# Kernel tuning notes

Hardware: AMD Instinct MI355X
Metric: run time of the kernel (lower is better)

The kernel has to match this reference:

```python
import jax, jax.numpy as jnp
import numpy as np

T, B = 32, 64
D_IN = 512      # input_size == embedding dim
H = 512         # hidden_size
V = 32000       # n_vocab
F_FEAT = 768    # feature_size
NH = 8          # num_heads
HD = H // NH    # head_dim


def setup_inputs() -> dict:
    key = jax.random.key(0)
    ks = jax.random.split(key, 16)
    s = 0.02
    inp = {
        'y': jax.random.randint(ks[0], (T, B), 0, V),
        'ctx': jax.random.normal(ks[1], (1, B, F_FEAT), jnp.float32),
        'emb_W': jax.random.normal(ks[2], (V, D_IN), jnp.float32) * s,
        # GRUCell dec0: gates ordered (r, z, n) as in torch
        'W_ih': jax.random.normal(ks[3], (3 * H, D_IN), jnp.float32) * s,
        'b_ih': jnp.zeros((3 * H,), jnp.float32),
        'W_hh': jax.random.normal(ks[4], (3 * H, H), jnp.float32) * s,
        'b_hh': jnp.zeros((3 * H,), jnp.float32),
        # FF att: feature_size -> hidden, tanh
        'W_att': jax.random.normal(ks[5], (H, F_FEAT), jnp.float32) * s,
        'b_att': jnp.zeros((H,), jnp.float32),
        # MultiHeadSelfAttention projections (hidden -> hidden)
        'Wq': jax.random.normal(ks[6], (H, H), jnp.float32) * s,
        'bq': jnp.zeros((H,), jnp.float32),
        'Wk': jax.random.normal(ks[7], (H, H), jnp.float32) * s,
        'bk': jnp.zeros((H,), jnp.float32),
        'Wv': jax.random.normal(ks[8], (H, H), jnp.float32) * s,
        'bv': jnp.zeros((H,), jnp.float32),
        'Wfc': jax.random.normal(ks[9], (H, H), jnp.float32) * s,
        'bfc': jnp.zeros((H,), jnp.float32),
        # FF hid2out: hidden -> input, tanh, bias_zero
        'W_h2o': jax.random.normal(ks[10], (D_IN, H), jnp.float32) * s,
        'b_h2o': jnp.zeros((D_IN,), jnp.float32),
        # FF out2prob: input -> vocab, linear
        'W_out': jax.random.normal(ks[11], (V, D_IN), jnp.float32) * s,
        'b_out': jnp.zeros((V,), jnp.float32),
    }
    return inp


def reference(y, ctx, emb_W, W_ih, b_ih, W_hh, b_hh, W_att, b_att,
              Wq, bq, Wk, bk, Wv, bv, Wfc, bfc, W_h2o, b_h2o, W_out, b_out):
    y_emb = emb_W[y]                                   # [T, B, D_IN]
    # ct is constant across decode steps: tanh FF over pooled image feature
    ct = jnp.tanh(ctx[0] @ W_att.T + b_att)            # [B, H]
    h0 = jnp.zeros((y.shape[1], H), y_emb.dtype)       # dec_init 'zero'

    def step(h, y_t):
        # torch GRUCell (gate order r, z, n)
        gi = y_t @ W_ih.T + b_ih                       # [B, 3H]
        gh = h @ W_hh.T + b_hh                         # [B, 3H]
        gi_r, gi_z, gi_n = jnp.split(gi, 3, axis=-1)
        gh_r, gh_z, gh_n = jnp.split(gh, 3, axis=-1)
        r = jax.nn.sigmoid(gi_r + gh_r)
        z = jax.nn.sigmoid(gi_z + gh_z)
        n = jnp.tanh(gi_n + r * gh_n)
        h1 = (1.0 - z) * n + z * h                     # [B, H]

        x = h1 * ct                                    # [B, H]
        # MultiHeadSelfAttention on a single vector, heads act as sequence
        q = (x @ Wq.T + bq).reshape(-1, NH, HD)        # [B, NH, HD]
        k = (x @ Wk.T + bk).reshape(-1, NH, HD)
        v = (x @ Wv.T + bv).reshape(-1, NH, HD)
        scores = jnp.einsum('bhd,bgd->bhg', q, k) / HD  # note: /head_dim (not sqrt)
        attw = jax.nn.softmax(scores, axis=-1)
        att_out = jnp.einsum('bhg,bgd->bhd', attw, v).reshape(-1, H)
        h2 = att_out @ Wfc.T + bfc                     # [B, H] (fc_out, vocab_size==H)

        logit = jnp.tanh(h2 @ W_h2o.T + b_h2o)         # [B, D_IN]
        prob = jax.nn.softmax(logit @ W_out.T + b_out, axis=-1)  # [B, V]
        return h1, prob                                # f_next returns h1 as next state

    _, probs = jax.lax.scan(step, h0, y_emb)           # [T, B, V]
    return probs
```

## Files before the change

kernel.cpp:

```cpp
#include <hip/hip_runtime.h>
#include <hip/hip_bf16.h>
#include <math.h>

typedef __bf16 bf16_t;
typedef __bf16 bf16x8 __attribute__((ext_vector_type(8)));
typedef __bf16 bf16x4 __attribute__((ext_vector_type(4)));
typedef float  f32x4  __attribute__((ext_vector_type(4)));

#define T_STEPS 32
#define BATCH   64
#define DIN     512
#define HID     512
#define VOCAB   32000
#define FFEAT   768
#define ROWS    2048
#define G3      1536
#define NBLK_A  32

#define EPI_F32  0
#define EPI_BF16 1
#define EPI_TANH 2
#define EPI_SUM  3
#define EPI_PROB 4

#define GLOAD16(gp, lp) __builtin_amdgcn_global_load_lds( \
    (const __attribute__((address_space(1))) void*)(gp),  \
    (__attribute__((address_space(3))) void*)(lp), 16, 0, 0)

template<int EPI>
__global__ __launch_bounds__(256) void gemm_lds(
    const bf16_t* __restrict__ A, const bf16_t* __restrict__ B,
    const float* __restrict__ bias, void* __restrict__ out,
    float* __restrict__ partial, const float* __restrict__ rowsum,
    int M, int N, int K, int NB)
{
  __shared__ bf16_t As[3][128 * 32];
  __shared__ bf16_t Bs[3][128 * 32];
  __shared__ float psum[128][2];

  const int lane = threadIdx.x & 63;
  const int wv   = threadIdx.x >> 6;
  const int wm = wv >> 1, wn = wv & 1;
  int bn, bm;
  if constexpr (EPI == EPI_SUM || EPI == EPI_PROB) {
    const int lin = blockIdx.x;
    const int nwg = NB * 16;
    const int cpx = nwg >> 3;
    const int wg  = (lin & 7) * cpx + (lin >> 3);
    bn = wg >> 4; bm = wg & 15;
  } else {
    bn = blockIdx.x; bm = blockIdx.y;
  }
  const int la = lane & 15, lg = lane >> 4;
  const int tid = threadIdx.x;

  auto stage = [&](int buf, int k0) {
#pragma unroll
    for (int q = 0; q < 2; ++q) {
      const int idx = q * 256 + tid;
      const int row = idx >> 2, c = idx & 3;
      const int gch = c ^ ((row >> 1) & 3);
      GLOAD16(A + (size_t)(bm * 128 + row) * K + k0 + gch * 8, &As[buf][idx * 8]);
      GLOAD16(B + (size_t)(bn * 128 + row) * K + k0 + gch * 8, &Bs[buf][idx * 8]);
    }
  };

  const int rdch = (lg ^ ((la >> 1) & 3)) * 8;

  f32x4 acc[4][4] = {};
  const int NT = K >> 5;
  stage(0, 0);
  stage(1, 32);
  for (int kt = 0; kt < NT; ++kt) {
    if (kt + 1 < NT) {
      asm volatile("s_waitcnt vmcnt(4)" ::: "memory");
    } else {
      asm volatile("s_waitcnt vmcnt(0)" ::: "memory");
    }
    __builtin_amdgcn_s_barrier();
    __builtin_amdgcn_sched_barrier(0);
    if (kt + 2 < NT) {
      int b2 = kt + 2; b2 -= (b2 >= 3) ? 3 : 0; b2 -= (b2 >= 3) ? 3 : 0;
      stage((kt + 2) % 3, (kt + 2) * 32);
      (void)b2;
    }
    const bf16_t* Ab = As[kt % 3];
    const bf16_t* Bb = Bs[kt % 3];
    bf16x8 a[4], b[4];
#pragma unroll
    for (int i = 0; i < 4; ++i)
      a[i] = *(const bf16x8*)(Ab + (wm * 64 + i * 16 + la) * 32 + rdch);
#pragma unroll
    for (int j = 0; j < 4; ++j)
      b[j] = *(const bf16x8*)(Bb + (wn * 64 + j * 16 + la) * 32 + rdch);
    __builtin_amdgcn_s_setprio(1);
#pragma unroll
    for (int i = 0; i < 4; ++i)
#pragma unroll
      for (int j = 0; j < 4; ++j)
        acc[i][j] = __builtin_amdgcn_mfma_f32_16x16x32_bf16(a[i], b[j], acc[i][j], 0, 0, 0);
    __builtin_amdgcn_s_setprio(0);
  }

  const int m0 = bm * 128 + wm * 64;
  const int n0 = bn * 128 + wn * 64;
  float bv4[4];
#pragma unroll
  for (int j = 0; j < 4; ++j) bv4[j] = bias[n0 + j * 16 + la];
#pragma unroll
  for (int i = 0; i < 4; ++i) {
#pragma unroll
    for (int r = 0; r < 4; ++r) {
      const int row = m0 + i * 16 + lg * 4 + r;
      float vsum = 0.f;
      float inv;
      if constexpr (EPI == EPI_PROB) inv = 1.0f / rowsum[row];
#pragma unroll
      for (int j = 0; j < 4; ++j) {
        const int col = n0 + j * 16 + la;
        float v = acc[i][j][r] + bv4[j];
        if constexpr (EPI == EPI_F32) {
          ((float*)out)[(size_t)row * N + col] = v;
        } else if constexpr (EPI == EPI_BF16) {
          ((bf16_t*)out)[(size_t)row * N + col] = (bf16_t)v;
        } else if constexpr (EPI == EPI_TANH) {
          ((bf16_t*)out)[(size_t)row * N + col] = (bf16_t)tanhf(v);
        } else if constexpr (EPI == EPI_SUM) {
          vsum += expf(v);
        } else {
          ((float*)out)[(size_t)row * N + col] = expf(v) * inv;
        }
      }
      if constexpr (EPI == EPI_SUM) {
        vsum += __shfl_xor(vsum, 1);
        vsum += __shfl_xor(vsum, 2);
        vsum += __shfl_xor(vsum, 4);
        vsum += __shfl_xor(vsum, 8);
        if (la == 0) psum[wm * 64 + i * 16 + lg * 4 + r][wn] = vsum;
      }
    }
  }
  if constexpr (EPI == EPI_SUM) {
    __syncthreads();
    if (tid < 128) {
      const int rb = bm * 128 + tid;
      partial[(size_t)rb * NB + bn] = psum[tid][0] + psum[tid][1];
    }
  }
  (void)partial; (void)rowsum; (void)NB;
}

__global__ __launch_bounds__(256) void phaseA_k(
    const bf16_t* __restrict__ Wg, const float* __restrict__ bhh,
    const float* __restrict__ gi, const float* __restrict__ ct,
    unsigned int* __restrict__ hbuf ,
    bf16_t* __restrict__ Xall, int* __restrict__ flags )
{
  __shared__ bf16_t Wl[48 * 520];
  __shared__ float bl[48];
  const int tid = threadIdx.x, blk = blockIdx.x;

  for (int i = tid; i < 48 * 64; i += 256) {
    const int rw = i >> 6, ch = (i & 63) << 3;
    *(bf16x8*)(Wl + rw * 520 + ch) = *(const bf16x8*)(Wg + (size_t)(blk * 48 + rw) * 512 + ch);
  }
  if (tid < 48) bl[tid] = bhh[blk * 48 + tid];
  __syncthreads();

  const int lane = tid & 63, wv = tid >> 6;
  const int la = lane & 15, lg = lane >> 4;
  const int jcol = blk * 16 + la;
  const int rowA = wv * 16 + la;

  const float blr = bl[la], blz = bl[16 + la], bln = bl[32 + la];
  float hprev[4], ctv[4];
#pragma unroll
  for (int r = 0; r < 4; ++r) {
    hprev[r] = 0.f;
    ctv[r] = ct[(size_t)(wv * 16 + lg * 4 + r) * HID + jcol];
  }

  for (int t = 0; t < T_STEPS; ++t) {
    const float* girow = gi + (size_t)t * BATCH * G3 + (size_t)blk * 48;
    float gv[12];
#pragma unroll
    for (int r = 0; r < 4; ++r) {
      const float* gp = girow + (size_t)(wv * 16 + lg * 4 + r) * G3;
      gv[r * 3 + 0] = gp[la];
      gv[r * 3 + 1] = gp[16 + la];
      gv[r * 3 + 2] = gp[32 + la];
    }
    if (t > 0) {
      if (lane < 32) {
        while (__hip_atomic_load(&flags[(lane * 4 + wv) * 16], __ATOMIC_RELAXED,
                                 __HIP_MEMORY_SCOPE_AGENT) < t)
          __builtin_amdgcn_s_sleep(1);
      }
      asm volatile("" ::: "memory");
    }
    const unsigned long long* hb =
        (const unsigned long long*)(hbuf + (size_t)(t & 1) * 16384);
    bf16x8 af[16];
#pragma unroll
    for (int q = 0; q < 16; ++q) {
      union { unsigned long long u[2]; bf16x8 v; } c;
      const size_t bidx = (size_t)(2 * q + (lg >> 1)) * 256 + rowA * 4 + (lg & 1) * 2;
      c.u[0] = __hip_atomic_load(hb + bidx,     __ATOMIC_RELAXED, __HIP_MEMORY_SCOPE_AGENT);
      c.u[1] = __hip_atomic_load(hb + bidx + 1, __ATOMIC_RELAXED, __HIP_MEMORY_SCOPE_AGENT);
      af[q] = c.v;
    }
    f32x4 acc0 = {}, acc1 = {}, acc2 = {};
#pragma unroll
    for (int q = 0; q < 16; ++q) {
      const bf16_t* wp = Wl + q * 32 + lg * 8;
      bf16x8 b0 = *(const bf16x8*)(wp + (0 * 16 + la) * 520);
      bf16x8 b1 = *(const bf16x8*)(wp + (1 * 16 + la) * 520);
      bf16x8 b2 = *(const bf16x8*)(wp + (2 * 16 + la) * 520);
      acc0 = __builtin_amdgcn_mfma_f32_16x16x32_bf16(af[q], b0, acc0, 0, 0, 0);
      acc1 = __builtin_amdgcn_mfma_f32_16x16x32_bf16(af[q], b1, acc1, 0, 0, 0);
      acc2 = __builtin_amdgcn_mfma_f32_16x16x32_bf16(af[q], b2, acc2, 0, 0, 0);
    }
    float h1v[4];
#pragma unroll
    for (int r = 0; r < 4; ++r) {
      const float ghr = acc0[r] + blr;
      const float ghz = acc1[r] + blz;
      const float ghn = acc2[r] + bln;
      const float rr = 1.f / (1.f + expf(-(gv[r * 3 + 0] + ghr)));
      const float zz = 1.f / (1.f + expf(-(gv[r * 3 + 1] + ghz)));
      const float nn = tanhf(gv[r * 3 + 2] + rr * ghn);
      h1v[r] = (1.f - zz) * nn + zz * hprev[r];
      hprev[r] = h1v[r];
    }
    unsigned int* hn = hbuf + (size_t)((t + 1) & 1) * 16384 + blk * 512;
#pragma unroll
    for (int r = 0; r < 4; ++r) {
      const int row = wv * 16 + lg * 4 + r;
      const unsigned int mine =
          (unsigned int)__builtin_bit_cast(unsigned short, (bf16_t)h1v[r]);
      const unsigned int other = (unsigned int)__shfl_xor((int)mine, 1);
      if ((la & 1) == 0) {
        __hip_atomic_store(hn + row * 8 + (la >> 1), mine | (other << 16),
                           __ATOMIC_RELAXED, __HIP_MEMORY_SCOPE_AGENT);
      }
    }
    asm volatile("s_waitcnt vmcnt(0)" ::: "memory");
    if (lane == 0) {
      __hip_atomic_store(&flags[(blk * 4 + wv) * 16], t + 1, __ATOMIC_RELAXED,
                         __HIP_MEMORY_SCOPE_AGENT);
    }
#pragma unroll
    for (int r = 0; r < 4; ++r) {
      const int row = wv * 16 + lg * 4 + r;
      Xall[((size_t)t * BATCH + row) * HID + jcol] = (bf16_t)(h1v[r] * ctv[r]);
    }
  }
}

__global__ __launch_bounds__(256) void attn_k(const bf16_t* __restrict__ QKV,
                                              bf16_t* __restrict__ attO)
{
  __shared__ float sq[4][512], sk[4][512], sv[4][512], sw[4][64];
  const int tid = threadIdx.x;
  const int wv = tid >> 6, lane = tid & 63;
  const int row = blockIdx.x * 4 + wv;
  const bf16_t* base = QKV + (size_t)row * G3;
  bf16x8 vq = *(const bf16x8*)(base + lane * 8);
  bf16x8 vk = *(const bf16x8*)(base + 512 + lane * 8);
  bf16x8 vv = *(const bf16x8*)(base + 1024 + lane * 8);
#pragma unroll
  for (int e = 0; e < 8; ++e) {
    sq[wv][lane * 8 + e] = (float)vq[e];
    sk[wv][lane * 8 + e] = (float)vk[e];
    sv[wv][lane * 8 + e] = (float)vv[e];
  }
  __syncthreads();
  const int h = lane >> 3, g = lane & 7;
  float s = 0.f;
#pragma unroll 16
  for (int d = 0; d < 64; ++d) s += sq[wv][h * 64 + d] * sk[wv][g * 64 + d];
  s *= (1.f / 64.f);
  float m = s;
  m = fmaxf(m, __shfl_xor(m, 1));
  m = fmaxf(m, __shfl_xor(m, 2));
  m = fmaxf(m, __shfl_xor(m, 4));
  const float e = expf(s - m);
  float sum = e;
  sum += __shfl_xor(sum, 1);
  sum += __shfl_xor(sum, 2);
  sum += __shfl_xor(sum, 4);
  sw[wv][lane] = e / sum;
  __syncthreads();
#pragma unroll
  for (int rep = 0; rep < 8; ++rep) {
    const int idx = rep * 64 + lane;
    const int hh = idx >> 6, d = idx & 63;
    float o = 0.f;
#pragma unroll
    for (int gg = 0; gg < 8; ++gg) o += sw[wv][hh * 8 + gg] * sv[wv][gg * 64 + d];
    attO[(size_t)row * HID + idx] = (bf16_t)o;
  }
}

__global__ __launch_bounds__(256) void cast_k(const float* __restrict__ src,
                                              bf16_t* __restrict__ dst, int n4)
{
  const int i = blockIdx.x * 256 + threadIdx.x;
  if (i >= n4) return;
  float4 v = ((const float4*)src)[i];
  bf16x4 o = {(bf16_t)v.x, (bf16_t)v.y, (bf16_t)v.z, (bf16_t)v.w};
  *(bf16x4*)(dst + (size_t)i * 4) = o;
}

__global__ __launch_bounds__(256) void perm_cast_k(const float* __restrict__ src,
                                                   bf16_t* __restrict__ dst)
{
  const int i = blockIdx.x * 256 + threadIdx.x;
  const int pg = i >> 7, kq = (i & 127) << 2;
  const int g = pg / 48, rem = pg - g * 48, sec = rem >> 4, jj = rem & 15;
  const int srow = sec * 512 + g * 16 + jj;
  float4 v = *(const float4*)(src + (size_t)srow * DIN + kq);
  bf16x4 o = {(bf16_t)v.x, (bf16_t)v.y, (bf16_t)v.z, (bf16_t)v.w};
  *(bf16x4*)(dst + (size_t)pg * DIN + kq) = o;
}

__global__ void perm_bias_k(const float* __restrict__ bih, const float* __restrict__ bhh,
                            float* __restrict__ bihp, float* __restrict__ bhhp)
{
  const int pg = blockIdx.x * 256 + threadIdx.x;
  if (pg >= G3) return;
  const int g = pg / 48, rem = pg - g * 48, sec = rem >> 4, jj = rem & 15;
  const int srow = sec * 512 + g * 16 + jj;
  bihp[pg] = bih[srow];
  bhhp[pg] = bhh[srow];
}

__global__ void bcat_k(const float* __restrict__ a, const float* __restrict__ b,
                       const float* __restrict__ c, float* __restrict__ d)
{
  const int i = blockIdx.x * 256 + threadIdx.x;
  if (i >= G3) return;
  d[i] = i < 512 ? a[i] : (i < 1024 ? b[i - 512] : c[i - 1024]);
}

__global__ __launch_bounds__(256) void yemb_k(const int* __restrict__ y,
                                              const float* __restrict__ embW,
                                              bf16_t* __restrict__ out)
{
  const int idx = blockIdx.x * 256 + threadIdx.x;
  const int rb = idx >> 6, c = (idx & 63) << 3;
  const int tok = y[rb];
  const float4* s = (const float4*)(embW + (size_t)tok * DIN + c);
  float4 v0 = s[0], v1 = s[1];
  bf16x8 o = {(bf16_t)v0.x, (bf16_t)v0.y, (bf16_t)v0.z, (bf16_t)v0.w,
              (bf16_t)v1.x, (bf16_t)v1.y, (bf16_t)v1.z, (bf16_t)v1.w};
  *(bf16x8*)(out + (size_t)rb * DIN + c) = o;
}

__global__ __launch_bounds__(256) void ct_k(const float* __restrict__ ctx,
                                            const float* __restrict__ Watt,
                                            const float* __restrict__ batt,
                                            float* __restrict__ ct)
{
  const int idx = blockIdx.x * 256 + threadIdx.x;
  const int b = idx >> 9, j = idx & 511;
  const float4* c4 = (const float4*)(ctx + (size_t)b * FFEAT);
  const float4* w4 = (const float4*)(Watt + (size_t)j * FFEAT);
  float s = batt[j];
  for (int q = 0; q < FFEAT / 4; ++q) {
    float4 cc = c4[q], ww = w4[q];
    s += cc.x * ww.x + cc.y * ww.y + cc.z * ww.z + cc.w * ww.w;
  }
  ct[idx] = tanhf(s);
}

__global__ __launch_bounds__(256) void reduce_rows(const float* __restrict__ partial,
                                                   float* __restrict__ rowsum, int NB)
{
  const int wv = threadIdx.x >> 6, lane = threadIdx.x & 63;
  const int row = blockIdx.x * 4 + wv;
  float s = 0.f;
  for (int c = lane; c < NB; c += 64) s += partial[(size_t)row * NB + c];
  for (int m = 1; m < 64; m <<= 1) s += __shfl_xor(s, m);
  if (lane == 0) rowsum[row] = s;
}

extern "C" void kernel_launch(void* const* d_in, const int* in_sizes, int n_in,
                              void* d_out, int out_size, void* d_ws, size_t ws_size,
                              hipStream_t stream)
{
  const int*   y     = (const int*)  d_in[0];
  const float* ctx   = (const float*)d_in[1];
  const float* embW  = (const float*)d_in[2];
  const float* W_ih  = (const float*)d_in[3];
  const float* b_ih  = (const float*)d_in[4];
  const float* W_hh  = (const float*)d_in[5];
  const float* b_hh  = (const float*)d_in[6];
  const float* W_att = (const float*)d_in[7];
  const float* b_att = (const float*)d_in[8];
  const float* Wq    = (const float*)d_in[9];
  const float* bq    = (const float*)d_in[10];
  const float* Wk    = (const float*)d_in[11];
  const float* bk    = (const float*)d_in[12];
  const float* Wv    = (const float*)d_in[13];
  const float* bv    = (const float*)d_in[14];
  const float* Wfc   = (const float*)d_in[15];
  const float* bfc   = (const float*)d_in[16];
  const float* Wh2o  = (const float*)d_in[17];
  const float* bh2o  = (const float*)d_in[18];
  const float* W_out = (const float*)d_in[19];
  const float* b_out = (const float*)d_in[20];

  char* p = (char*)d_ws;
  auto alloc = [&](size_t bytes) {
    char* r = p;
    p += (bytes + 255) & ~(size_t)255;
    return r;
  };
  bf16_t* WoutB   = (bf16_t*)alloc((size_t)VOCAB * DIN * 2);
  bf16_t* WgIh    = (bf16_t*)alloc((size_t)G3 * DIN * 2);
  bf16_t* WgHh    = (bf16_t*)alloc((size_t)G3 * DIN * 2);
  bf16_t* Wqkv    = (bf16_t*)alloc((size_t)G3 * DIN * 2);
  bf16_t* WfcB    = (bf16_t*)alloc((size_t)HID * HID * 2);
  bf16_t* Wh2oB   = (bf16_t*)alloc((size_t)HID * HID * 2);
  float*  bIhP    = (float*)alloc(G3 * 4);
  float*  bHhP    = (float*)alloc(G3 * 4);
  float*  bQkv    = (float*)alloc(G3 * 4);
  bf16_t* Yemb    = (bf16_t*)alloc((size_t)ROWS * DIN * 2);
  float*  giP     = (float*)alloc((size_t)ROWS * G3 * 4);
  float*  ctB     = (float*)alloc((size_t)BATCH * HID * 4);
  unsigned int* hbuf = (unsigned int*)alloc((size_t)2 * 16384 * 4);
  bf16_t* Xall    = (bf16_t*)alloc((size_t)ROWS * DIN * 2);
  bf16_t* QKV     = (bf16_t*)alloc((size_t)ROWS * G3 * 2);
  bf16_t* attO    = (bf16_t*)alloc((size_t)ROWS * HID * 2);
  bf16_t* h2B     = (bf16_t*)alloc((size_t)ROWS * HID * 2);
  bf16_t* logit   = (bf16_t*)alloc((size_t)ROWS * DIN * 2);
  float*  partial = (float*)alloc((size_t)ROWS * 250 * 4);
  float*  rowsum  = (float*)alloc((size_t)ROWS * 4);
  int*    flags   = (int*)alloc(32 * 4 * 64);

  hipMemsetAsync(hbuf, 0, (size_t)2 * 16384 * 4, stream);
  hipMemsetAsync(flags, 0, 32 * 4 * 64, stream);

  cast_k<<<(VOCAB * DIN / 4 + 255) / 256, 256, 0, stream>>>(W_out, WoutB, VOCAB * DIN / 4);
  cast_k<<<256, 256, 0, stream>>>(Wq, Wqkv, HID * HID / 4);
  cast_k<<<256, 256, 0, stream>>>(Wk, Wqkv + (size_t)HID * DIN, HID * HID / 4);
  cast_k<<<256, 256, 0, stream>>>(Wv, Wqkv + (size_t)2 * HID * DIN, HID * HID / 4);
  cast_k<<<256, 256, 0, stream>>>(Wfc, WfcB, HID * HID / 4);
  cast_k<<<256, 256, 0, stream>>>(Wh2o, Wh2oB, HID * HID / 4);
  perm_cast_k<<<768, 256, 0, stream>>>(W_ih, WgIh);
  perm_cast_k<<<768, 256, 0, stream>>>(W_hh, WgHh);
  perm_bias_k<<<6, 256, 0, stream>>>(b_ih, b_hh, bIhP, bHhP);
  bcat_k<<<6, 256, 0, stream>>>(bq, bk, bv, bQkv);
  yemb_k<<<512, 256, 0, stream>>>(y, embW, Yemb);
  ct_k<<<128, 256, 0, stream>>>(ctx, W_att, b_att, ctB);

  gemm_lds<EPI_F32><<<dim3(12, 16), 256, 0, stream>>>(
      Yemb, WgIh, bIhP, giP, nullptr, nullptr, ROWS, G3, DIN, 12);

  phaseA_k<<<NBLK_A, 256, 0, stream>>>(WgHh, bHhP, giP, ctB, hbuf, Xall, flags);

  gemm_lds<EPI_BF16><<<dim3(12, 16), 256, 0, stream>>>(
      Xall, Wqkv, bQkv, QKV, nullptr, nullptr, ROWS, G3, DIN, 12);

  attn_k<<<512, 256, 0, stream>>>(QKV, attO);

  gemm_lds<EPI_BF16><<<dim3(4, 16), 256, 0, stream>>>(
      attO, WfcB, bfc, h2B, nullptr, nullptr, ROWS, HID, HID, 4);

  gemm_lds<EPI_TANH><<<dim3(4, 16), 256, 0, stream>>>(
      h2B, Wh2oB, bh2o, logit, nullptr, nullptr, ROWS, DIN, HID, 4);

  gemm_lds<EPI_SUM><<<dim3(250 * 16), 256, 0, stream>>>(
      logit, WoutB, b_out, nullptr, partial, nullptr, ROWS, VOCAB, DIN, 250);
  reduce_rows<<<512, 256, 0, stream>>>(partial, rowsum, 250);
  gemm_lds<EPI_PROB><<<dim3(250 * 16), 256, 0, stream>>>(
      logit, WoutB, b_out, d_out, nullptr, rowsum, ROWS, VOCAB, DIN, 250);
}
```

Baseline: 504.4 us.

## Use 256x256-tile 8-wave GEMM for vocab projection and overlap W_out cast

Adds a new gemm_v kernel with 256x256 output tiles, 512 threads, and a 64-deep K double-buffered LDS pipeline split into eight sub-phases. It is used for the two vocab-sized passes (exp-sum and normalized prob write) to raise arithmetic intensity and cut repeated loads of logit and W_out. The W_out fp32-to-bf16 cast moves into extra blocks of the sequential GRU recurrence kernel, so it runs on CUs that recurrence leaves idle. Risks include lower occupancy from the larger LDS footprint, and interference between the cast blocks and the latency-sensitive recurrence blocks.

```diff
diff --git a/kernel.cpp b/kernel.cpp
--- a/kernel.cpp
+++ b/kernel.cpp
@@ -27,30 +27,170 @@
     (const __attribute__((address_space(1))) void*)(gp),  \
     (__attribute__((address_space(3))) void*)(lp), 16, 0, 0)
 
+#define PHASEV(BUF, MH, NH, STAGE_STMT, GATE_STMT)                            \
+  {                                                                           \
+    bf16x8 af_[8], bf_[4];                                                    \
+    _Pragma("unroll")                                                         \
+    for (int m2 = 0; m2 < 4; ++m2) {                                          \
+      const int row = wm * 64 + m2 * 16 + la;                                 \
+      _Pragma("unroll")                                                       \
+      for (int ks = 0; ks < 2; ++ks) {                                        \
+        const int sl = (ks * 4 + lg) ^ (row & 7);                             \
+        af_[m2 * 2 + ks] =                                                    \
+            *(const bf16x8*)&lds[((BUF)*4 + (MH)) * 8192 + row * 64 + sl * 8];\
+      }                                                                       \
+    }                                                                         \
+    _Pragma("unroll")                                                         \
+    for (int n2 = 0; n2 < 2; ++n2) {                                          \
+      const int row = wn * 32 + n2 * 16 + la;                                 \
+      _Pragma("unroll")                                                       \
+      for (int ks = 0; ks < 2; ++ks) {                                        \
+        const int sl = (ks * 4 + lg) ^ (row & 7);                             \
+        bf_[n2 * 2 + ks] =                                                    \
+            *(const bf16x8*)&lds[((BUF)*4 + 2 + (NH)) * 8192 + row * 64 + sl * 8];\
+      }                                                                       \
+    }                                                                         \
+    STAGE_STMT;                                                               \
+    GATE_STMT;                                                                \
+    __builtin_amdgcn_s_barrier();                                             \
+    __builtin_amdgcn_s_setprio(1);                                            \
+    _Pragma("unroll")                                                         \
+    for (int m2 = 0; m2 < 4; ++m2)                                            \
+      _Pragma("unroll")                                                       \
+      for (int n2 = 0; n2 < 2; ++n2)                                          \
+        _Pragma("unroll")                                                     \
+        for (int ks = 0; ks < 2; ++ks)                                        \
+          acc[(MH)*4 + m2][(NH)*2 + n2] =                                     \
+              __builtin_amdgcn_mfma_f32_16x16x32_bf16(                        \
+                  af_[m2*2+ks], bf_[n2*2+ks],                                 \
+                  acc[(MH)*4 + m2][(NH)*2 + n2], 0, 0, 0);                    \
+    __builtin_amdgcn_s_setprio(0);                                            \
+    __builtin_amdgcn_s_barrier();                                             \
+  }
+
+template<int EPI>
+__global__ __launch_bounds__(512, 2) void gemm_v(
+    const bf16_t* __restrict__ A, const bf16_t* __restrict__ B,
+    const float* __restrict__ bias, float* __restrict__ out,
+    float* __restrict__ partial, const float* __restrict__ rowsum,
+    int M, int N, int K, int NB)
+{
+  __shared__ bf16_t lds[2 * 4 * 8192];
+  __shared__ float psum[256][4];
+  const int tid = threadIdx.x;
+  const int lane = tid & 63, wv = tid >> 6;
+  const int wm = wv >> 2, wn = wv & 3;
+  const int la = lane & 15, lg = lane >> 4;
+
+  const int lin = blockIdx.x;
+  const int mt = M >> 8;
+  const int cpx = (NB * mt) >> 3;
+  const int wg = (lin & 7) * cpx + (lin >> 3);
+  const int bn = wg / mt, bm = wg - bn * mt;
+
+  auto stageA = [&](int buf, int h, int kt) {
+    const size_t base = (size_t)(bm * 256 + h * 128) * K + (size_t)kt * 64;
+#pragma unroll
+    for (int q = 0; q < 2; ++q) {
+      const int L = q * 512 + tid;
+      const int row = L >> 3, sl = L & 7;
+      const int c = sl ^ (row & 7);
+      GLOAD16(A + base + (size_t)row * K + c * 8,
+              &lds[(buf * 4 + h) * 8192 + L * 8]);
+    }
+  };
+  auto stageB = [&](int buf, int h, int kt) {
+    const size_t base = (size_t)(bn * 256 + h * 128) * K + (size_t)kt * 64;
+#pragma unroll
+    for (int q = 0; q < 2; ++q) {
+      const int L = q * 512 + tid;
+      const int row = L >> 3, sl = L & 7;
+      const int c = sl ^ (row & 7);
+      GLOAD16(B + base + (size_t)row * K + c * 8,
+              &lds[(buf * 4 + 2 + h) * 8192 + L * 8]);
+    }
+  };
+
+  f32x4 acc[8][4] = {};
+  const int NITER = K >> 7;
+
+  stageA(0, 0, 0); stageB(0, 0, 0); stageA(0, 1, 0); stageB(0, 1, 0);
+  stageA(1, 0, 1); stageB(1, 0, 1);
+  asm volatile("s_waitcnt vmcnt(4)" ::: "memory");
+  __builtin_amdgcn_s_barrier();
+
+  for (int it = 0; it < NITER; ++it) {
+    const int t0 = 2 * it;
+    const bool lastI = (it == NITER - 1);
+    PHASEV(0, 0, 0, { stageA(1, 1, t0 + 1); }, ;)
+    PHASEV(0, 0, 1, { stageB(1, 1, t0 + 1); }, ;)
+    PHASEV(0, 1, 0, { if (!lastI) stageA(0, 0, t0 + 2); }, ;)
+    PHASEV(0, 1, 1, { if (!lastI) stageB(0, 0, t0 + 2); },
+           { if (lastI) { asm volatile("s_waitcnt vmcnt(0)" ::: "memory"); }
+             else       { asm volatile("s_waitcnt vmcnt(4)" ::: "memory"); } })
+    PHASEV(1, 0, 0, { if (!lastI) stageA(0, 1, t0 + 2); }, ;)
+    PHASEV(1, 0, 1, { if (!lastI) stageB(0, 1, t0 + 2); }, ;)
+    PHASEV(1, 1, 0, { if (!lastI) stageA(1, 0, t0 + 3); }, ;)
+    PHASEV(1, 1, 1, { if (!lastI) stageB(1, 0, t0 + 3); },
+           { if (!lastI) { asm volatile("s_waitcnt vmcnt(4)" ::: "memory"); } })
+  }
+
+  float bv[4];
+#pragma unroll
+  for (int nj = 0; nj < 4; ++nj) {
+    const int col = bn * 256 + (nj >> 1) * 128 + wn * 32 + (nj & 1) * 16 + la;
+    bv[nj] = bias[col];
+  }
+#pragma unroll
+  for (int mi = 0; mi < 8; ++mi) {
+#pragma unroll
+    for (int rr = 0; rr < 4; ++rr) {
+      const int rowl = (mi >> 2) * 128 + wm * 64 + (mi & 3) * 16 + lg * 4 + rr;
+      const int row = bm * 256 + rowl;
+      float vsum = 0.f, inv;
+      if constexpr (EPI == EPI_PROB) inv = 1.0f / rowsum[row];
+#pragma unroll
+      for (int nj = 0; nj < 4; ++nj) {
+        const float v = acc[mi][nj][rr] + bv[nj];
+        if constexpr (EPI == EPI_SUM) {
+          vsum += expf(v);
+        } else {
+          const int col = bn * 256 + (nj >> 1) * 128 + wn * 32 + (nj & 1) * 16 + la;
+          out[(size_t)row * N + col] = expf(v) * inv;
+        }
+      }
+      if constexpr (EPI == EPI_SUM) {
+        vsum += __shfl_xor(vsum, 1);
+        vsum += __shfl_xor(vsum, 2);
+        vsum += __shfl_xor(vsum, 4);
+        vsum += __shfl_xor(vsum, 8);
+        if (la == 0) psum[rowl][wn] = vsum;
+      }
+    }
+  }
+  if constexpr (EPI == EPI_SUM) {
+    __syncthreads();
+    if (tid < 256) {
+      partial[(size_t)(bm * 256 + tid) * NB + bn] =
+          psum[tid][0] + psum[tid][1] + psum[tid][2] + psum[tid][3];
+    }
+  }
+  (void)out; (void)partial; (void)rowsum;
+}
+
 template<int EPI>
 __global__ __launch_bounds__(256) void gemm_lds(
     const bf16_t* __restrict__ A, const bf16_t* __restrict__ B,
     const float* __restrict__ bias, void* __restrict__ out,
-    float* __restrict__ partial, const float* __restrict__ rowsum,
-    int M, int N, int K, int NB)
+    int M, int N, int K)
 {
   __shared__ bf16_t As[3][128 * 32];
   __shared__ bf16_t Bs[3][128 * 32];
-  __shared__ float psum[128][2];
 
   const int lane = threadIdx.x & 63;
   const int wv   = threadIdx.x >> 6;
   const int wm = wv >> 1, wn = wv & 1;
-  int bn, bm;
-  if constexpr (EPI == EPI_SUM || EPI == EPI_PROB) {
-    const int lin = blockIdx.x;
-    const int nwg = NB * 16;
-    const int cpx = nwg >> 3;
-    const int wg  = (lin & 7) * cpx + (lin >> 3);
-    bn = wg >> 4; bm = wg & 15;
-  } else {
-    bn = blockIdx.x; bm = blockIdx.y;
-  }
+  const int bn = blockIdx.x, bm = blockIdx.y;
   const int la = lane & 15, lg = lane >> 4;
   const int tid = threadIdx.x;
 
@@ -64,7 +204,6 @@
       GLOAD16(B + (size_t)(bn * 128 + row) * K + k0 + gch * 8, &Bs[buf][idx * 8]);
     }
   };
-
   const int rdch = (lg ^ ((la >> 1) & 3)) * 8;
 
   f32x4 acc[4][4] = {};
@@ -79,11 +218,7 @@
     }
     __builtin_amdgcn_s_barrier();
     __builtin_amdgcn_sched_barrier(0);
-    if (kt + 2 < NT) {
-      int b2 = kt + 2; b2 -= (b2 >= 3) ? 3 : 0; b2 -= (b2 >= 3) ? 3 : 0;
-      stage((kt + 2) % 3, (kt + 2) * 32);
-      (void)b2;
-    }
+    if (kt + 2 < NT) stage((kt + 2) % 3, (kt + 2) * 32);
     const bf16_t* Ab = As[kt % 3];
     const bf16_t* Bb = Bs[kt % 3];
     bf16x8 a[4], b[4];
@@ -112,9 +247,6 @@
 #pragma unroll
     for (int r = 0; r < 4; ++r) {
       const int row = m0 + i * 16 + lg * 4 + r;
-      float vsum = 0.f;
-      float inv;
-      if constexpr (EPI == EPI_PROB) inv = 1.0f / rowsum[row];
 #pragma unroll
       for (int j = 0; j < 4; ++j) {
         const int col = n0 + j * 16 + la;
@@ -123,42 +255,35 @@
           ((float*)out)[(size_t)row * N + col] = v;
         } else if constexpr (EPI == EPI_BF16) {
           ((bf16_t*)out)[(size_t)row * N + col] = (bf16_t)v;
-        } else if constexpr (EPI == EPI_TANH) {
+        } else {
           ((bf16_t*)out)[(size_t)row * N + col] = (bf16_t)tanhf(v);
-        } else if constexpr (EPI == EPI_SUM) {
-          vsum += expf(v);
-        } else {
-          ((float*)out)[(size_t)row * N + col] = expf(v) * inv;
         }
       }
-      if constexpr (EPI == EPI_SUM) {
-        vsum += __shfl_xor(vsum, 1);
-        vsum += __shfl_xor(vsum, 2);
-        vsum += __shfl_xor(vsum, 4);
-        vsum += __shfl_xor(vsum, 8);
-        if (la == 0) psum[wm * 64 + i * 16 + lg * 4 + r][wn] = vsum;
-      }
-    }
-  }
-  if constexpr (EPI == EPI_SUM) {
-    __syncthreads();
-    if (tid < 128) {
-      const int rb = bm * 128 + tid;
-      partial[(size_t)rb * NB + bn] = psum[tid][0] + psum[tid][1];
-    }
-  }
-  (void)partial; (void)rowsum; (void)NB;
+    }
+  }
 }
 
 __global__ __launch_bounds__(256) void phaseA_k(
     const bf16_t* __restrict__ Wg, const float* __restrict__ bhh,
     const float* __restrict__ gi, const float* __restrict__ ct,
-    unsigned int* __restrict__ hbuf ,
-    bf16_t* __restrict__ Xall, int* __restrict__ flags )
+    unsigned int* __restrict__ hbuf, bf16_t* __restrict__ Xall,
+    int* __restrict__ flags, const float* __restrict__ Wout_f32,
+    bf16_t* __restrict__ WoutB)
 {
   __shared__ bf16_t Wl[48 * 520];
   __shared__ float bl[48];
   const int tid = threadIdx.x, blk = blockIdx.x;
+
+  if (blk >= NBLK_A) {
+    const int NCB = gridDim.x - NBLK_A;
+    const int n4 = VOCAB * DIN / 4;
+    for (int i = (blk - NBLK_A) * 256 + tid; i < n4; i += NCB * 256) {
+      float4 v = ((const float4*)Wout_f32)[i];
+      bf16x4 o = {(bf16_t)v.x, (bf16_t)v.y, (bf16_t)v.z, (bf16_t)v.w};
+      *(bf16x4*)(WoutB + (size_t)i * 4) = o;
+    }
+    return;
+  }
 
   for (int i = tid; i < 48 * 64; i += 256) {
     const int rw = i >> 6, ch = (i & 63) << 3;
@@ -442,7 +567,6 @@
   hipMemsetAsync(hbuf, 0, (size_t)2 * 16384 * 4, stream);
   hipMemsetAsync(flags, 0, 32 * 4 * 64, stream);
 
-  cast_k<<<(VOCAB * DIN / 4 + 255) / 256, 256, 0, stream>>>(W_out, WoutB, VOCAB * DIN / 4);
   cast_k<<<256, 256, 0, stream>>>(Wq, Wqkv, HID * HID / 4);
   cast_k<<<256, 256, 0, stream>>>(Wk, Wqkv + (size_t)HID * DIN, HID * HID / 4);
   cast_k<<<256, 256, 0, stream>>>(Wv, Wqkv + (size_t)2 * HID * DIN, HID * HID / 4);
@@ -456,24 +580,25 @@
   ct_k<<<128, 256, 0, stream>>>(ctx, W_att, b_att, ctB);
 
   gemm_lds<EPI_F32><<<dim3(12, 16), 256, 0, stream>>>(
-      Yemb, WgIh, bIhP, giP, nullptr, nullptr, ROWS, G3, DIN, 12);
-
-  phaseA_k<<<NBLK_A, 256, 0, stream>>>(WgHh, bHhP, giP, ctB, hbuf, Xall, flags);
+      Yemb, WgIh, bIhP, giP, ROWS, G3, DIN);
+
+  phaseA_k<<<224, 256, 0, stream>>>(WgHh, bHhP, giP, ctB, hbuf, Xall, flags,
+                                    W_out, WoutB);
 
   gemm_lds<EPI_BF16><<<dim3(12, 16), 256, 0, stream>>>(
-      Xall, Wqkv, bQkv, QKV, nullptr, nullptr, ROWS, G3, DIN, 12);
+      Xall, Wqkv, bQkv, QKV, ROWS, G3, DIN);
 
   attn_k<<<512, 256, 0, stream>>>(QKV, attO);
 
   gemm_lds<EPI_BF16><<<dim3(4, 16), 256, 0, stream>>>(
-      attO, WfcB, bfc, h2B, nullptr, nullptr, ROWS, HID, HID, 4);
+      attO, WfcB, bfc, h2B, ROWS, HID, HID);
 
   gemm_lds<EPI_TANH><<<dim3(4, 16), 256, 0, stream>>>(
-      h2B, Wh2oB, bh2o, logit, nullptr, nullptr, ROWS, DIN, HID, 4);
-
-  gemm_lds<EPI_SUM><<<dim3(250 * 16), 256, 0, stream>>>(
-      logit, WoutB, b_out, nullptr, partial, nullptr, ROWS, VOCAB, DIN, 250);
-  reduce_rows<<<512, 256, 0, stream>>>(partial, rowsum, 250);
-  gemm_lds<EPI_PROB><<<dim3(250 * 16), 256, 0, stream>>>(
-      logit, WoutB, b_out, d_out, nullptr, rowsum, ROWS, VOCAB, DIN, 250);
-}
+      h2B, Wh2oB, bh2o, logit, ROWS, DIN, HID);
+
+  gemm_v<EPI_SUM><<<1000, 512, 0, stream>>>(
+      logit, WoutB, b_out, nullptr, partial, nullptr, ROWS, VOCAB, DIN, 125);
+  reduce_rows<<<512, 256, 0, stream>>>(partial, rowsum, 125);
+  gemm_v<EPI_PROB><<<1000, 512, 0, stream>>>(
+      logit, WoutB, b_out, (float*)d_out, nullptr, rowsum, ROWS, VOCAB, DIN, 125);
+}
```

Result: faster. 492.1 us (-2.5%).
